# Optimization experiments

Hardware: AMD Instinct MI355X
Metric: run time of the kernel (lower is better)

The kernel has to match this reference:

```python
import jax, jax.numpy as jnp
import numpy as np

N_NODES = 50000
N_EDGES = 800000
D_IN = 64
D_OUT = 64


def setup_inputs() -> dict:
    key = jax.random.key(0)
    k1, k2, k3, k4, k5, k6 = jax.random.split(key, 6)
    feat = jax.random.normal(k1, (N_NODES, D_IN), dtype=jnp.float32)
    edge_weight = jax.random.uniform(k2, (N_EDGES, 1), dtype=jnp.float32)
    # xavier_uniform bound for [D_IN, D_OUT]
    bound = float(np.sqrt(6.0 / (D_IN + D_OUT)))
    W1 = jax.random.uniform(k3, (D_IN, D_OUT), minval=-bound, maxval=bound, dtype=jnp.float32)
    W2 = jax.random.uniform(k4, (D_IN, D_OUT), minval=-bound, maxval=bound, dtype=jnp.float32)
    src = jax.random.randint(k5, (N_EDGES,), 0, N_NODES, dtype=jnp.int64)
    dst = jax.random.randint(k6, (N_EDGES,), 0, N_NODES, dtype=jnp.int64)
    return {"feat": feat, "edge_weight": edge_weight, "W1": W1, "W2": W2, "src": src, "dst": dst}


def reference(feat, edge_weight, W1, W2, src, dst):
    # message: u_sub_e -> src feature minus (broadcast) edge weight  [E, D_IN]
    msgs = feat[src] - edge_weight
    # sum aggregation over destination nodes  [N, D_IN]
    agg = jax.ops.segment_sum(msgs, dst, num_segments=feat.shape[0])
    # dual dense projections; no activation (activation=None)
    rst = jnp.matmul(feat, W1) + jnp.matmul(agg, W2)
    return rst
```

## Files before the change

### kernel.cpp

```cpp
#include <hip/hip_runtime.h>

#define NN 50000
#define NE 800000
#define D  64
#define NB 196
#define EBLK 2048
#define NEB 391
#define CAPB 4608
#define CONVB 1563

typedef unsigned int u32;
typedef unsigned short u16;
typedef unsigned long long u64;
typedef __attribute__((ext_vector_type(8))) short bf16x8;
typedef __attribute__((ext_vector_type(4))) float f32x4;
typedef __attribute__((ext_vector_type(2))) float f32x2;

__device__ __forceinline__ int wave_incl_scan(int v, int lane) {
    #pragma unroll
    for (int off = 1; off < 64; off <<= 1) {
        int t = __shfl_up(v, off);
        if (lane >= off) v += t;
    }
    return v;
}

__device__ __forceinline__ u32 f2bf(float x) {
    u32 u = __float_as_uint(x);
    return (u + 0x7fffu + ((u >> 16) & 1u)) >> 16;
}

__device__ __forceinline__ bf16x8 as_bf8(uint4 u) {
    union { uint4 a; bf16x8 b; } x; x.a = u; return x.b;
}

__device__ __forceinline__ u32 pk_fp8x4(float a, float b, float c, float d) {
    int w = __builtin_amdgcn_cvt_pk_fp8_f32(a, b, 0, false);
    w = __builtin_amdgcn_cvt_pk_fp8_f32(c, d, w, true);
    return (u32)w;
}

__global__ __launch_bounds__(256) void convz_kernel(const float* __restrict__ feat,
                                                    uint4* __restrict__ featb,
                                                    uint2* __restrict__ featb8,
                                                    u32* __restrict__ cursor)
{
    int tid = threadIdx.x;
    if (blockIdx.x == CONVB) {
        if (tid < NB) cursor[tid] = 0;
        return;
    }
    int i = blockIdx.x * 256 + tid;
    if (i >= NN * D / 8) return;
    const float4* f4 = (const float4*)feat;
    float4 a = f4[2 * i], b = f4[2 * i + 1];
    uint4 o;
    o.x = f2bf(a.x) | (f2bf(a.y) << 16);
    o.y = f2bf(a.z) | (f2bf(a.w) << 16);
    o.z = f2bf(b.x) | (f2bf(b.y) << 16);
    o.w = f2bf(b.z) | (f2bf(b.w) << 16);
    featb[i] = o;
    uint2 p8;
    p8.x = pk_fp8x4(a.x, a.y, a.z, a.w);
    p8.y = pk_fp8x4(b.x, b.y, b.z, b.w);
    featb8[i] = p8;
}

__global__ __launch_bounds__(256) void kb_scatter(const int* __restrict__ src,
                                                  const int* __restrict__ dst,
                                                  const float* __restrict__ ew,
                                                  u32* __restrict__ cursor,
                                                  u64* __restrict__ sorted)
{
    __shared__ u32 h[NB], eb[NB], ctr[NB], gb[NB];
    __shared__ u64 buf[EBLK];
    int tid = threadIdx.x;
    if (tid < NB) h[tid] = 0;
    __syncthreads();
    int base = blockIdx.x * EBLK;
    int n = min(EBLK, NE - base);
    for (int k = tid; k < n; k += 256)
        atomicAdd(&h[((u32)dst[base + k]) >> 8], 1u);
    __syncthreads();
    if (tid < 64) {
        u32 carry = 0;
        for (int c = 0; c < 4; ++c) {
            int idx = c * 64 + tid;
            u32 v = (idx < NB) ? h[idx] : 0;
            int incl = wave_incl_scan((int)v, tid);
            if (idx < NB) { u32 e = (u32)incl - v + carry; eb[idx] = e; ctr[idx] = e; }
            carry += (u32)__shfl(incl, 63);
        }
    }
    if (tid < NB) gb[tid] = atomicAdd(&cursor[tid], h[tid]);
    __syncthreads();
    for (int k = tid; k < n; k += 256) {
        int e = base + k;
        u32 d = (u32)dst[e], s = (u32)src[e];
        u64 rec = ((u64)((d << 16) | s) << 32) | (u64)__float_as_uint(ew[e]);
        u32 p = atomicAdd(&ctr[d >> 8], 1u);
        buf[p] = rec;
    }
    __syncthreads();
    for (int k = tid; k < n; k += 256) {
        u64 rec = buf[k];
        u32 bin = (u32)(rec >> 56);
        u32 idx = gb[bin] + (u32)k - eb[bin];
        if (idx < CAPB) sorted[(size_t)bin * CAPB + idx] = rec;
    }
}

__global__ __launch_bounds__(256) void kc_nodesort(const u64* __restrict__ sorted,
                                                   const u32* __restrict__ cursor,
                                                   u16* __restrict__ srcs16,
                                                   u32* __restrict__ nodeStart2,
                                                   float* __restrict__ sW)
{
    __shared__ u32 hcnt[256], hbase[257], ctr[256];
    __shared__ u64 buf[CAPB];
    int tid = threadIdx.x;
    int bin = blockIdx.x;
    int n = min((int)cursor[bin], CAPB);
    const size_t rbase = (size_t)bin * CAPB;

    hcnt[tid] = 0;
    __syncthreads();
    for (int k = tid; k < n; k += 256)
        atomicAdd(&hcnt[(int)(sorted[rbase + k] >> 48) & 255], 1u);
    __syncthreads();
    if (tid < 64) {
        u32 carry = 0;
        for (int c = 0; c < 4; ++c) {
            int idx = c * 64 + tid;
            u32 v = hcnt[idx];
            int incl = wave_incl_scan((int)v, tid);
            u32 ex = (u32)incl - v + carry;
            hbase[idx] = ex; ctr[idx] = ex;
            carry += (u32)__shfl(incl, 63);
        }
        if (tid == 63) hbase[256] = carry;
    }
    __syncthreads();
    for (int k = tid; k < n; k += 256) {
        u64 rec = sorted[rbase + k];
        u32 p = atomicAdd(&ctr[(int)(rec >> 48) & 255], 1u);
        buf[p] = rec;
    }
    __syncthreads();
    for (int k = tid; k < n; k += 256)
        srcs16[rbase + k] = (u16)(buf[k] >> 32);
    nodeStart2[bin * 257 + tid] = (u32)rbase + hbase[tid];
    if (tid == 0) nodeStart2[bin * 257 + 256] = (u32)rbase + hbase[256];
    {
        int node = (bin << 8) + tid;
        if (node < NN) {
            float s = 0.f;
            for (int j = (int)hbase[tid]; j < (int)hbase[tid + 1]; ++j)
                s += __uint_as_float((u32)buf[j]);
            sW[node] = s;
        }
    }
}

__global__ __launch_bounds__(256) void k4_gather(const u32* __restrict__ fb8,
                                                 const u16* __restrict__ srcs16,
                                                 const u32* __restrict__ nodeStart2,
                                                 uint2* __restrict__ aggb)
{
    int wv   = (blockIdx.x * 256 + threadIdx.x) >> 6;
    int lane = threadIdx.x & 63;
    int g    = lane >> 4;
    int li   = lane & 15;
    int node = wv * 4 + g;
    if (node >= NN) return;
    int bin = node >> 8, ln = node & 255;

    int e   = (int)nodeStart2[bin * 257 + ln];
    int end = (int)nodeStart2[bin * 257 + ln + 1];

    float4 acc = make_float4(0.f, 0.f, 0.f, 0.f);
    for (; e + 7 < end; e += 8) {
        int s0 = srcs16[e],     s1 = srcs16[e + 1];
        int s2 = srcs16[e + 2], s3 = srcs16[e + 3];
        int s4 = srcs16[e + 4], s5 = srcs16[e + 5];
        int s6 = srcs16[e + 6], s7 = srcs16[e + 7];
        u32 u0 = fb8[(size_t)s0 * 16 + li];
        u32 u1 = fb8[(size_t)s1 * 16 + li];
        u32 u2 = fb8[(size_t)s2 * 16 + li];
        u32 u3 = fb8[(size_t)s3 * 16 + li];
        u32 u4 = fb8[(size_t)s4 * 16 + li];
        u32 u5 = fb8[(size_t)s5 * 16 + li];
        u32 u6 = fb8[(size_t)s6 * 16 + li];
        u32 u7 = fb8[(size_t)s7 * 16 + li];
        #pragma unroll
        for (int j = 0; j < 8; ++j) {
            u32 uu = j == 0 ? u0 : j == 1 ? u1 : j == 2 ? u2 : j == 3 ? u3
                   : j == 4 ? u4 : j == 5 ? u5 : j == 6 ? u6 : u7;
            f32x2 lo = __builtin_amdgcn_cvt_pk_f32_fp8((int)uu, false);
            f32x2 hi = __builtin_amdgcn_cvt_pk_f32_fp8((int)uu, true);
            acc.x += lo.x; acc.y += lo.y; acc.z += hi.x; acc.w += hi.y;
        }
    }
    for (; e < end; ++e) {
        u32 uu = fb8[(size_t)srcs16[e] * 16 + li];
        f32x2 lo = __builtin_amdgcn_cvt_pk_f32_fp8((int)uu, false);
        f32x2 hi = __builtin_amdgcn_cvt_pk_f32_fp8((int)uu, true);
        acc.x += lo.x; acc.y += lo.y; acc.z += hi.x; acc.w += hi.y;
    }

    uint2 o;
    o.x = f2bf(acc.x) | (f2bf(acc.y) << 16);
    o.y = f2bf(acc.z) | (f2bf(acc.w) << 16);
    aggb[(size_t)node * 16 + li] = o;
}

__global__ __launch_bounds__(256) void gemm_mfma(
    const uint4* __restrict__ featb,
    const uint4* __restrict__ aggb,
    const float* __restrict__ sW,
    const float* __restrict__ W1,
    const float* __restrict__ W2,
    float* __restrict__ out)
{
    __shared__ u16 wT[64][136];
    __shared__ float csp[4][64];
    __shared__ float csum[64];
    const int tid = threadIdx.x;

    for (int i = tid; i < 8192; i += 256) {
        int k = i >> 6, c = i & 63;
        float v = (k < 64) ? W1[i] : W2[i - 4096];
        wT[c][k] = (u16)f2bf(v);
    }
    {
        int c = tid & 63, kq = tid >> 6;
        float s = 0.f;
        for (int k = kq * 16; k < kq * 16 + 16; ++k) s += W2[k * 64 + c];
        csp[kq][c] = s;
    }
    __syncthreads();
    if (tid < 64) csum[tid] = csp[0][tid] + csp[1][tid] + csp[2][tid] + csp[3][tid];
    __syncthreads();

    int gw = blockIdx.x * 4 + (tid >> 6);
    if (gw >= NN / 16) return;
    const int l  = tid & 63;
    const int lr = l & 15;
    const int q  = l >> 4;

    bf16x8 b[4][4];
    #pragma unroll
    for (int nt = 0; nt < 4; ++nt)
        #pragma unroll
        for (int kk = 0; kk < 4; ++kk)
            b[nt][kk] = *(const bf16x8*)&wT[nt * 16 + lr][kk * 32 + q * 8];

    const int m0 = gw * 16;
    const size_t arow = (size_t)(m0 + lr) * 8;
    bf16x8 a0 = as_bf8(featb[arow + q]);
    bf16x8 a1 = as_bf8(featb[arow + 4 + q]);
    bf16x8 a2 = as_bf8(aggb[arow + q]);
    bf16x8 a3 = as_bf8(aggb[arow + 4 + q]);

    f32x4 acc0 = {0.f, 0.f, 0.f, 0.f};
    f32x4 acc1 = acc0, acc2 = acc0, acc3 = acc0;

    acc0 = __builtin_amdgcn_mfma_f32_16x16x32_bf16(a0, b[0][0], acc0, 0, 0, 0);
    acc1 = __builtin_amdgcn_mfma_f32_16x16x32_bf16(a0, b[1][0], acc1, 0, 0, 0);
    acc2 = __builtin_amdgcn_mfma_f32_16x16x32_bf16(a0, b[2][0], acc2, 0, 0, 0);
    acc3 = __builtin_amdgcn_mfma_f32_16x16x32_bf16(a0, b[3][0], acc3, 0, 0, 0);

    acc0 = __builtin_amdgcn_mfma_f32_16x16x32_bf16(a1, b[0][1], acc0, 0, 0, 0);
    acc1 = __builtin_amdgcn_mfma_f32_16x16x32_bf16(a1, b[1][1], acc1, 0, 0, 0);
    acc2 = __builtin_amdgcn_mfma_f32_16x16x32_bf16(a1, b[2][1], acc2, 0, 0, 0);
    acc3 = __builtin_amdgcn_mfma_f32_16x16x32_bf16(a1, b[3][1], acc3, 0, 0, 0);

    acc0 = __builtin_amdgcn_mfma_f32_16x16x32_bf16(a2, b[0][2], acc0, 0, 0, 0);
    acc1 = __builtin_amdgcn_mfma_f32_16x16x32_bf16(a2, b[1][2], acc1, 0, 0, 0);
    acc2 = __builtin_amdgcn_mfma_f32_16x16x32_bf16(a2, b[2][2], acc2, 0, 0, 0);
    acc3 = __builtin_amdgcn_mfma_f32_16x16x32_bf16(a2, b[3][2], acc3, 0, 0, 0);

    acc0 = __builtin_amdgcn_mfma_f32_16x16x32_bf16(a3, b[0][3], acc0, 0, 0, 0);
    acc1 = __builtin_amdgcn_mfma_f32_16x16x32_bf16(a3, b[1][3], acc1, 0, 0, 0);
    acc2 = __builtin_amdgcn_mfma_f32_16x16x32_bf16(a3, b[2][3], acc2, 0, 0, 0);
    acc3 = __builtin_amdgcn_mfma_f32_16x16x32_bf16(a3, b[3][3], acc3, 0, 0, 0);

    float4 sw4 = *(const float4*)&sW[m0 + q * 4];
    const float* swp = (const float*)&sw4;

    #pragma unroll
    for (int r = 0; r < 4; ++r) {
        size_t rowoff = (size_t)(m0 + q * 4 + r) * D;
        float s = swp[r];
        out[rowoff +  0 + lr] = acc0[r] - s * csum[ 0 + lr];
        out[rowoff + 16 + lr] = acc1[r] - s * csum[16 + lr];
        out[rowoff + 32 + lr] = acc2[r] - s * csum[32 + lr];
        out[rowoff + 48 + lr] = acc3[r] - s * csum[48 + lr];
    }
}

extern "C" void kernel_launch(void* const* d_in, const int* in_sizes, int n_in,
                              void* d_out, int out_size, void* d_ws, size_t ws_size,
                              hipStream_t stream)
{
    const float* feat = (const float*)d_in[0];
    const float* ew   = (const float*)d_in[1];
    const float* W1   = (const float*)d_in[2];
    const float* W2   = (const float*)d_in[3];
    const int*   src  = (const int*)  d_in[4];
    const int*   dst  = (const int*)  d_in[5];
    float* out = (float*)d_out;

    char* p = (char*)d_ws;
    size_t o = 0;
    auto take = [&](size_t bytes) { char* q = p + o; o = (o + bytes + 255) & ~(size_t)255; return q; };
    u64* sorted     = (u64*)take((size_t)NB * CAPB * 8);
    u16* srcs16     = (u16*)take((size_t)NB * CAPB * 2);
    u32* cursor     = (u32*)take((size_t)NB * 4);
    u32* nodeStart2 = (u32*)take((size_t)NB * 257 * 4);
    uint4* featb    = (uint4*)take((size_t)NN * D * 2);
    uint2* featb8   = (uint2*)take((size_t)NN * D);
    uint4* aggb     = (uint4*)take((size_t)NN * D * 2);
    float* sW       = (float*)take((size_t)NN * 4 + 256);

    convz_kernel<<<CONVB + 1, 256, 0, stream>>>(feat, featb, featb8, cursor);
    kb_scatter  <<<NEB, 256, 0, stream>>>(src, dst, ew, cursor, sorted);
    kc_nodesort <<<NB, 256, 0, stream>>>(sorted, cursor, srcs16, nodeStart2, sW);
    k4_gather   <<<(NN + 15) / 16, 256, 0, stream>>>((const u32*)featb8, srcs16,
                                                     nodeStart2, (uint2*)aggb);
    gemm_mfma   <<<(NN / 16 + 3) / 4, 256, 0, stream>>>(featb, aggb, sW, W1, W2, out);
}
```

Before: 64.31 us.

## Merge feature conversion into edge scatter and shrink sorted records

```diff
diff --git a/kernel.cpp b/kernel.cpp
--- a/kernel.cpp
+++ b/kernel.cpp
@@ -40,41 +40,38 @@
     return (u32)w;
 }
 
-__global__ __launch_bounds__(256) void convz_kernel(const float* __restrict__ feat,
-                                                    uint4* __restrict__ featb,
-                                                    uint2* __restrict__ featb8,
-                                                    u32* __restrict__ cursor)
-{
-    int tid = threadIdx.x;
-    if (blockIdx.x == CONVB) {
-        if (tid < NB) cursor[tid] = 0;
-        return;
-    }
-    int i = blockIdx.x * 256 + tid;
-    if (i >= NN * D / 8) return;
-    const float4* f4 = (const float4*)feat;
-    float4 a = f4[2 * i], b = f4[2 * i + 1];
-    uint4 o;
-    o.x = f2bf(a.x) | (f2bf(a.y) << 16);
-    o.y = f2bf(a.z) | (f2bf(a.w) << 16);
-    o.z = f2bf(b.x) | (f2bf(b.y) << 16);
-    o.w = f2bf(b.z) | (f2bf(b.w) << 16);
-    featb[i] = o;
-    uint2 p8;
-    p8.x = pk_fp8x4(a.x, a.y, a.z, a.w);
-    p8.y = pk_fp8x4(b.x, b.y, b.z, b.w);
-    featb8[i] = p8;
-}
-
-__global__ __launch_bounds__(256) void kb_scatter(const int* __restrict__ src,
-                                                  const int* __restrict__ dst,
-                                                  const float* __restrict__ ew,
-                                                  u32* __restrict__ cursor,
-                                                  u64* __restrict__ sorted)
+__global__ __launch_bounds__(256) void kb_merged(const int* __restrict__ src,
+                                                 const int* __restrict__ dst,
+                                                 const float* __restrict__ ew,
+                                                 const float* __restrict__ feat,
+                                                 u32* __restrict__ cursor,
+                                                 u32* __restrict__ sortedR,
+                                                 u16* __restrict__ sortedW,
+                                                 uint4* __restrict__ featb,
+                                                 uint2* __restrict__ featb8)
 {
     __shared__ u32 h[NB], eb[NB], ctr[NB], gb[NB];
     __shared__ u64 buf[EBLK];
     int tid = threadIdx.x;
+
+    if (blockIdx.x >= NEB) {
+        int i = (blockIdx.x - NEB) * 256 + tid;
+        if (i >= NN * D / 8) return;
+        const float4* f4 = (const float4*)feat;
+        float4 a = f4[2 * i], b = f4[2 * i + 1];
+        uint4 o;
+        o.x = f2bf(a.x) | (f2bf(a.y) << 16);
+        o.y = f2bf(a.z) | (f2bf(a.w) << 16);
+        o.z = f2bf(b.x) | (f2bf(b.y) << 16);
+        o.w = f2bf(b.z) | (f2bf(b.w) << 16);
+        featb[i] = o;
+        uint2 p8;
+        p8.x = pk_fp8x4(a.x, a.y, a.z, a.w);
+        p8.y = pk_fp8x4(b.x, b.y, b.z, b.w);
+        featb8[i] = p8;
+        return;
+    }
+
     if (tid < NB) h[tid] = 0;
     __syncthreads();
     int base = blockIdx.x * EBLK;
@@ -97,27 +94,34 @@
     for (int k = tid; k < n; k += 256) {
         int e = base + k;
         u32 d = (u32)dst[e], s = (u32)src[e];
-        u64 rec = ((u64)((d << 16) | s) << 32) | (u64)__float_as_uint(ew[e]);
+        u64 rec = ((u64)d << 32) | ((u64)s << 16) | (u64)f2bf(ew[e]);
         u32 p = atomicAdd(&ctr[d >> 8], 1u);
         buf[p] = rec;
     }
     __syncthreads();
     for (int k = tid; k < n; k += 256) {
         u64 rec = buf[k];
-        u32 bin = (u32)(rec >> 56);
+        u32 bin = (u32)(rec >> 40);
         u32 idx = gb[bin] + (u32)k - eb[bin];
-        if (idx < CAPB) sorted[(size_t)bin * CAPB + idx] = rec;
-    }
-}
-
-__global__ __launch_bounds__(256) void kc_nodesort(const u64* __restrict__ sorted,
+        if (idx < CAPB) {
+            u32 dstl = (u32)(rec >> 32) & 255u;
+            u32 s    = (u32)(rec >> 16) & 0xffffu;
+            sortedR[(size_t)bin * CAPB + idx] = (dstl << 16) | s;
+            sortedW[(size_t)bin * CAPB + idx] = (u16)(rec & 0xffffu);
+        }
+    }
+}
+
+__global__ __launch_bounds__(256) void kc_nodesort(const u32* __restrict__ sortedR,
+                                                   const u16* __restrict__ sortedW,
                                                    const u32* __restrict__ cursor,
                                                    u16* __restrict__ srcs16,
                                                    u32* __restrict__ nodeStart2,
                                                    float* __restrict__ sW)
 {
     __shared__ u32 hcnt[256], hbase[257], ctr[256];
-    __shared__ u64 buf[CAPB];
+    __shared__ u16 bufR[CAPB];
+    __shared__ u16 bufW[CAPB];
     int tid = threadIdx.x;
     int bin = blockIdx.x;
     int n = min((int)cursor[bin], CAPB);
@@ -126,7 +130,7 @@
     hcnt[tid] = 0;
     __syncthreads();
     for (int k = tid; k < n; k += 256)
-        atomicAdd(&hcnt[(int)(sorted[rbase + k] >> 48) & 255], 1u);
+        atomicAdd(&hcnt[(sortedR[rbase + k] >> 16) & 255u], 1u);
     __syncthreads();
     if (tid < 64) {
         u32 carry = 0;
@@ -142,13 +146,15 @@
     }
     __syncthreads();
     for (int k = tid; k < n; k += 256) {
-        u64 rec = sorted[rbase + k];
-        u32 p = atomicAdd(&ctr[(int)(rec >> 48) & 255], 1u);
-        buf[p] = rec;
+        u32 r = sortedR[rbase + k];
+        u16 w = sortedW[rbase + k];
+        u32 p = atomicAdd(&ctr[(r >> 16) & 255u], 1u);
+        bufR[p] = (u16)(r & 0xffffu);
+        bufW[p] = w;
     }
     __syncthreads();
     for (int k = tid; k < n; k += 256)
-        srcs16[rbase + k] = (u16)(buf[k] >> 32);
+        srcs16[rbase + k] = bufR[k];
     nodeStart2[bin * 257 + tid] = (u32)rbase + hbase[tid];
     if (tid == 0) nodeStart2[bin * 257 + 256] = (u32)rbase + hbase[256];
     {
@@ -156,7 +162,7 @@
         if (node < NN) {
             float s = 0.f;
             for (int j = (int)hbase[tid]; j < (int)hbase[tid + 1]; ++j)
-                s += __uint_as_float((u32)buf[j]);
+                s += __uint_as_float((u32)bufW[j] << 16);
             sW[node] = s;
         }
     }
@@ -314,7 +320,8 @@
     char* p = (char*)d_ws;
     size_t o = 0;
     auto take = [&](size_t bytes) { char* q = p + o; o = (o + bytes + 255) & ~(size_t)255; return q; };
-    u64* sorted     = (u64*)take((size_t)NB * CAPB * 8);
+    u32* sortedR    = (u32*)take((size_t)NB * CAPB * 4);
+    u16* sortedW    = (u16*)take((size_t)NB * CAPB * 2);
     u16* srcs16     = (u16*)take((size_t)NB * CAPB * 2);
     u32* cursor     = (u32*)take((size_t)NB * 4);
     u32* nodeStart2 = (u32*)take((size_t)NB * 257 * 4);
@@ -323,10 +330,12 @@
     uint4* aggb     = (uint4*)take((size_t)NN * D * 2);
     float* sW       = (float*)take((size_t)NN * 4 + 256);
 
-    convz_kernel<<<CONVB + 1, 256, 0, stream>>>(feat, featb, featb8, cursor);
-    kb_scatter  <<<NEB, 256, 0, stream>>>(src, dst, ew, cursor, sorted);
-    kc_nodesort <<<NB, 256, 0, stream>>>(sorted, cursor, srcs16, nodeStart2, sW);
-    k4_gather   <<<(NN + 15) / 16, 256, 0, stream>>>((const u32*)featb8, srcs16,
-                                                     nodeStart2, (uint2*)aggb);
-    gemm_mfma   <<<(NN / 16 + 3) / 4, 256, 0, stream>>>(featb, aggb, sW, W1, W2, out);
-}
+    hipMemsetAsync(cursor, 0, (size_t)NB * 4, stream);
+    kb_merged  <<<NEB + CONVB, 256, 0, stream>>>(src, dst, ew, feat, cursor,
+                                                 sortedR, sortedW, featb, featb8);
+    kc_nodesort<<<NB, 256, 0, stream>>>(sortedR, sortedW, cursor, srcs16,
+                                        nodeStart2, sW);
+    k4_gather  <<<(NN + 15) / 16, 256, 0, stream>>>((const u32*)featb8, srcs16,
+                                                    nodeStart2, (uint2*)aggb);
+    gemm_mfma  <<<(NN / 16 + 3) / 4, 256, 0, stream>>>(featb, aggb, sW, W1, W2, out);
+}
```

New measurement: 65.36 us. Within noise of the previous version (+1.6%).
